# Optimization experiments

Hardware: AMD Instinct MI355X
Metric: run time of the kernel (lower is better)

Reference implementation:

```python
import jax, jax.numpy as jnp
import numpy as np

B, T, C = 4, 2048, 1024
H = 16
HD = C // H


def setup_inputs() -> dict:
    key = jax.random.key(0)
    k1, k2, k3 = jax.random.split(key, 3)
    x = jax.random.normal(k1, (B, T, C), dtype=jnp.float32)
    w_qkv = jax.random.normal(k2, (C, 3 * C), dtype=jnp.float32) * (C ** -0.5)
    w_proj = jax.random.normal(k3, (C, C), dtype=jnp.float32) * (C ** -0.5)
    b_proj = jnp.zeros((C,), dtype=jnp.float32)
    return {"x": x, "w_qkv": w_qkv, "w_proj": w_proj, "b_proj": b_proj}


def reference(x, w_qkv, w_proj, b_proj):
    Bd, Td, Cd = x.shape
    scale = HD ** -0.5
    qkv = x @ w_qkv  # [B,T,3C]
    q, k, v = jnp.split(qkv, 3, axis=-1)
    # [B,H,T,HD]
    q = q.reshape(Bd, Td, H, HD).transpose(0, 2, 1, 3)
    k = k.reshape(Bd, Td, H, HD).transpose(0, 2, 1, 3)
    v = v.reshape(Bd, Td, H, HD).transpose(0, 2, 1, 3)
    att = jnp.einsum('bhqd,bhkd->bhqk', q, k) * scale
    causal = jnp.triu(jnp.ones((Td, Td), dtype=bool), k=1)
    att = jnp.where(causal, -jnp.inf, att)
    att = jax.nn.softmax(att, axis=-1)
    y = jnp.einsum('bhqk,bhkd->bhqd', att, v)
    y = y.transpose(0, 2, 1, 3).reshape(Bd, Td, Cd)
    return y @ w_proj + b_proj
```

## Files before the change

kernel.cpp:

```cpp
#include <hip/hip_runtime.h>

typedef unsigned short u16;
typedef __attribute__((ext_vector_type(8))) short short8;
typedef __attribute__((ext_vector_type(4))) short short4v;
typedef __attribute__((ext_vector_type(4))) float floatx4;
typedef __attribute__((ext_vector_type(4))) unsigned short ushort4v;

#define B_ 4
#define T_ 2048
#define C_ 1024
#define H_ 16
#define HD_ 64

template <bool V> struct BC { static constexpr bool value = V; };

static __device__ __forceinline__ u16 f2bf(float f) {
  union { float f; unsigned int i; } c; c.f = f;
  unsigned int u = c.i;
  return (u16)((u + 0x7FFFu + ((u >> 16) & 1u)) >> 16);
}
static __device__ __forceinline__ unsigned pk2(float lo, float hi) {
  union { float f; unsigned u; } a, b; a.f = hi; b.f = lo;
  return __builtin_amdgcn_perm(a.u, b.u, 0x07060302u);
}
static __device__ __forceinline__ unsigned pk2r(float lo, float hi) {
  return (unsigned)f2bf(lo) | ((unsigned)f2bf(hi) << 16);
}

static __device__ __forceinline__ void gload16(const u16* g, u16* l) {
  __builtin_amdgcn_global_load_lds(
      (const __attribute__((address_space(1))) unsigned int*)(g),
      (__attribute__((address_space(3))) unsigned int*)(l), 16, 0, 0);
}

__global__ __launch_bounds__(256) void prep_k(const float* __restrict__ x,
                                              const float* __restrict__ w_qkv,
                                              const float* __restrict__ w_proj,
                                              u16* __restrict__ xbf,
                                              u16* __restrict__ wqkvT,
                                              u16* __restrict__ wprojT) {
  const int bid = blockIdx.x;
  if (bid < 8192) {
    const int i = bid * 256 + threadIdx.x;
    const float4 f = ((const float4*)x)[i];
    ushort4v o;
    o.x = f2bf(f.x); o.y = f2bf(f.y); o.z = f2bf(f.z); o.w = f2bf(f.w);
    *(ushort4v*)(xbf + (size_t)i * 4) = o;
    return;
  }
  __shared__ u16 tile[32][33];
  const float* in;
  u16* out;
  int R, Cc, tb;
  if (bid < 11264) {
    in = w_qkv; out = wqkvT; R = C_; Cc = 3 * C_; tb = bid - 8192;
  } else {
    in = w_proj; out = wprojT; R = C_; Cc = C_; tb = bid - 11264;
  }
  const int tpr = Cc / 32;
  const int bx = (tb % tpr) * 32;
  const int by = (tb / tpr) * 32;
  const int tx = threadIdx.x & 31;
  const int ty = threadIdx.x >> 5;
  #pragma unroll
  for (int i = ty; i < 32; i += 8)
    tile[i][tx] = f2bf(in[(size_t)(by + i) * Cc + bx + tx]);
  __syncthreads();
  #pragma unroll
  for (int i = ty; i < 32; i += 8)
    out[(size_t)(bx + i) * R + by + tx] = tile[tx][i];
}

template <int MODE, int NT>
__global__ __launch_bounds__(256) void gemm_bt(const u16* __restrict__ A,
                                               const u16* __restrict__ Bt,
                                               u16* __restrict__ outb,
                                               u16* __restrict__ outv,
                                               float* __restrict__ outf,
                                               const float* __restrict__ bias,
                                               int M, int N, int K) {
  __shared__ __align__(16) u16 lds[8192 + NT * 2048];
  const int bid = blockIdx.x;
  const int s = bid >> 3;
  const int tM = ((bid & 7) * 8 + (s & 7)) * 128;
  const int tN = (s >> 3) * (NT * 32);
  const int tid = threadIdx.x;
  const int wave = tid >> 6;
  const int lane = tid & 63;
  const int lr = lane & 15;
  const int quad = lane >> 4;
  const int wm = (wave >> 1) * 64;
  const int wn = (wave & 1) * (NT * 16);

  const int srow = lane >> 2;
  const int skofs = ((lane & 3) ^ ((lane >> 3) & 3)) * 8;

  const floatx4 zf = {0.f, 0.f, 0.f, 0.f};
  floatx4 acc[4][NT];
  #pragma unroll
  for (int i = 0; i < 4; i++)
    #pragma unroll
    for (int j = 0; j < NT; j++) acc[i][j] = zf;

  const int csw = (lr >> 1) & 3;

  for (int k0 = 0; k0 < K; k0 += 64) {
    __syncthreads();
    #pragma unroll
    for (int half = 0; half < 2; half++) {
      const int kk = k0 + half * 32;
      #pragma unroll
      for (int j = 0; j < 2; j++) {
        const int seg = wave * 2 + j;
        const int row = seg * 16 + srow;
        gload16(A + (size_t)(tM + row) * K + kk + skofs, &lds[half * 4096 + seg * 512]);
      }
      #pragma unroll
      for (int j = 0; j < NT / 2; j++) {
        const int seg = wave * (NT / 2) + j;
        const int row = seg * 16 + srow;
        gload16(Bt + (size_t)(tN + row) * K + kk + skofs,
                &lds[8192 + half * (NT * 1024) + seg * 512]);
      }
    }
    __syncthreads();

    #pragma unroll
    for (int half = 0; half < 2; half++) {
      short8 af[4], bfr[NT];
      #pragma unroll
      for (int mt = 0; mt < 4; mt++)
        af[mt] = *(const short8*)(&lds[half * 4096 + (wm + mt * 16 + lr) * 32 + ((quad ^ csw) * 8)]);
      #pragma unroll
      for (int nt = 0; nt < NT; nt++)
        bfr[nt] = *(const short8*)(&lds[8192 + half * (NT * 1024) + (wn + nt * 16 + lr) * 32 + ((quad ^ csw) * 8)]);
      #pragma unroll
      for (int mt = 0; mt < 4; mt++)
        #pragma unroll
        for (int nt = 0; nt < NT; nt++)
          acc[mt][nt] = __builtin_amdgcn_mfma_f32_16x16x32_bf16(af[mt], bfr[nt],
                                                                acc[mt][nt], 0, 0, 0);
    }
  }

  if (MODE == 1 && tN >= 2 * C_) {
    const int b = tM >> 11;
    const int t0 = tM & (T_ - 1);
    const int h0 = (tN - 2 * C_) >> 6;
    #pragma unroll
    for (int pass = 0; pass < 2; pass++) {
      __syncthreads();
      if ((wave & 1) == pass) {
        #pragma unroll
        for (int nt = 0; nt < NT; nt++) {
          const int nr = nt * 16 + lr;
          #pragma unroll
          for (int mt = 0; mt < 4; mt++) {
            const int mr = wm + mt * 16 + quad * 4;
            *(unsigned*)(&lds[nr * 136 + mr]) = pk2r(acc[mt][nt][0], acc[mt][nt][1]);
            *(unsigned*)(&lds[nr * 136 + mr + 2]) = pk2r(acc[mt][nt][2], acc[mt][nt][3]);
          }
        }
      }
      __syncthreads();
      const int bh = b * H_ + h0 + pass;
      u16* vbase = outv + (size_t)bh * HD_ * T_ + t0;
      #pragma unroll
      for (int i = 0; i < 4; i++) {
        const int c = tid + i * 256;
        const int nr = c >> 4, m8 = (c & 15) * 8;
        const short8 v = *(const short8*)(&lds[nr * 136 + m8]);
        *(short8*)(vbase + (size_t)nr * T_ + m8) = v;
      }
    }
    return;
  }

  #pragma unroll
  for (int mt = 0; mt < 4; mt++) {
    const int m0 = tM + wm + mt * 16 + quad * 4;
    #pragma unroll
    for (int nt = 0; nt < NT; nt++) {
      const int n = tN + wn + nt * 16 + lr;
      #pragma unroll
      for (int r = 0; r < 4; r++) {
        const float v = acc[mt][nt][r];
        const size_t m = (size_t)(m0 + r);
        if (MODE == 2) __builtin_nontemporal_store(v + bias[n], &outf[m * N + n]);
        else           outb[m * N + n] = f2bf(v);
      }
    }
  }
}

__global__ __launch_bounds__(256, 4) void attn_k(const u16* __restrict__ qkv,
                                                 const u16* __restrict__ vt,
                                                 u16* __restrict__ y) {
  __shared__ __align__(16) u16 Ks[64 * 64];
  __shared__ __align__(16) u16 Vs[64 * 64];
  const int bid = blockIdx.x;
  const int s = bid >> 3;
  const int qp = s >> 3;
  const int bh = ((s & 7) << 3) | (bid & 7);
  const int b = bh >> 4, h = bh & 15;
  const int tid = threadIdx.x;
  const int wave = tid >> 6;
  const int lane = tid & 63;
  const int lr = lane & 15;
  const int quad = lane >> 4;
  const int qtA = qp, qtB = 31 - qp;

  const int srow = lane >> 3;
  const int skofs = ((lane & 7) ^ ((lane >> 3) & 7)) * 8;
  const int gsw = lr & 7;

  const size_t RS = 3 * C_;
  const u16* qcol = qkv + (size_t)b * T_ * RS + h * HD_;
  const u16* kcol = qcol + C_;

  const size_t qrA = (size_t)(qtA * 64 + wave * 16 + lr) * RS;
  const size_t qrB = (size_t)(qtB * 64 + wave * 16 + lr) * RS;
  const short8 aq0A = *(const short8*)(qcol + qrA + quad * 8);
  const short8 aq1A = *(const short8*)(qcol + qrA + 32 + quad * 8);
  const short8 aq0B = *(const short8*)(qcol + qrB + quad * 8);
  const short8 aq1B = *(const short8*)(qcol + qrB + 32 + quad * 8);

  const floatx4 zf = {0.f, 0.f, 0.f, 0.f};
  const float C1 = 0.125f * 1.44269504f;
  const float C2 = -16.0f * 1.44269504f;
  const short8 vones = {16256, 16256, 16256, 16256, 16256, 16256, 16256, 16256};

  floatx4 accA[4], accB[4];
  floatx4 accSA = zf, accSB = zf;
  #pragma unroll
  for (int i = 0; i < 4; i++) { accA[i] = zf; accB[i] = zf; }

  auto stage = [&](int kt) {
    __syncthreads();
    #pragma unroll
    for (int j = 0; j < 2; j++) {
      const int seg = wave * 2 + j;
      const int row = seg * 8 + srow;
      gload16(kcol + (size_t)(kt * 64 + row) * RS + skofs, &Ks[seg * 512]);
      gload16(vt + ((size_t)bh * HD_ + row) * T_ + kt * 64 + skofs, &Vs[seg * 512]);
    }
    __syncthreads();
  };

  auto core = [&](auto WA, auto DA, auto DB) {
    constexpr bool wA = decltype(WA)::value;
    constexpr bool dA = decltype(DA)::value;
    constexpr bool dB = decltype(DB)::value;
    float peA[4][4], peB[4][4];
    #pragma unroll
    for (int nt = 0; nt < 4; nt++) {
      const short8 bk0 =
          *(const short8*)(&Ks[(nt * 16 + lr) * 64 + ((quad ^ gsw) * 8)]);
      const short8 bk1 =
          *(const short8*)(&Ks[(nt * 16 + lr) * 64 + (((quad + 4) ^ gsw) * 8)]);
      {
        floatx4 st = __builtin_amdgcn_mfma_f32_16x16x32_bf16(
            bk1, aq1B,
            __builtin_amdgcn_mfma_f32_16x16x32_bf16(bk0, aq0B, zf, 0, 0, 0),
            0, 0, 0);
        #pragma unroll
        for (int r = 0; r < 4; r++) {
          float pe = __builtin_amdgcn_exp2f(fmaf(st[r], C1, C2));
          if constexpr (dB)
            if (nt * 16 + quad * 4 + r > wave * 16 + lr) pe = 0.f;
          peB[nt][r] = pe;
        }
      }
      if constexpr (wA) {
        floatx4 st = __builtin_amdgcn_mfma_f32_16x16x32_bf16(
            bk1, aq1A,
            __builtin_amdgcn_mfma_f32_16x16x32_bf16(bk0, aq0A, zf, 0, 0, 0),
            0, 0, 0);
        #pragma unroll
        for (int r = 0; r < 4; r++) {
          float pe = __builtin_amdgcn_exp2f(fmaf(st[r], C1, C2));
          if constexpr (dA)
            if (nt * 16 + quad * 4 + r > wave * 16 + lr) pe = 0.f;
          peA[nt][r] = pe;
        }
      }
    }

    short8 pB[2], pA[2];
    #pragma unroll
    for (int h2 = 0; h2 < 2; h2++) {
      union { unsigned u[4]; short8 s8; } w;
      w.u[0] = pk2(peB[2 * h2][0], peB[2 * h2][1]);
      w.u[1] = pk2(peB[2 * h2][2], peB[2 * h2][3]);
      w.u[2] = pk2(peB[2 * h2 + 1][0], peB[2 * h2 + 1][1]);
      w.u[3] = pk2(peB[2 * h2 + 1][2], peB[2 * h2 + 1][3]);
      pB[h2] = w.s8;
    }
    if constexpr (wA) {
      #pragma unroll
      for (int h2 = 0; h2 < 2; h2++) {
        union { unsigned u[4]; short8 s8; } w;
        w.u[0] = pk2(peA[2 * h2][0], peA[2 * h2][1]);
        w.u[1] = pk2(peA[2 * h2][2], peA[2 * h2][3]);
        w.u[2] = pk2(peA[2 * h2 + 1][0], peA[2 * h2 + 1][1]);
        w.u[3] = pk2(peA[2 * h2 + 1][2], peA[2 * h2 + 1][3]);
        pA[h2] = w.s8;
      }
    }

    #pragma unroll
    for (int h2 = 0; h2 < 2; h2++) {
      accSB = __builtin_amdgcn_mfma_f32_16x16x32_bf16(vones, pB[h2], accSB, 0, 0, 0);
      if constexpr (wA)
        accSA = __builtin_amdgcn_mfma_f32_16x16x32_bf16(vones, pA[h2], accSA, 0, 0, 0);
      #pragma unroll
      for (int dt = 0; dt < 4; dt++) {
        const int base = (dt * 16 + lr) * 64;
        const int cl = h2 * 4 + (quad >> 1);
        const int off_lo = ((cl ^ gsw) * 8) + (quad & 1) * 4;
        const int off_hi = (((cl + 2) ^ gsw) * 8) + (quad & 1) * 4;
        const short4v vlo = *(const short4v*)(&Vs[base + off_lo]);
        const short4v vhi = *(const short4v*)(&Vs[base + off_hi]);
        const short8 av = __builtin_shufflevector(vlo, vhi, 0, 1, 2, 3, 4, 5, 6, 7);
        accB[dt] = __builtin_amdgcn_mfma_f32_16x16x32_bf16(av, pB[h2], accB[dt], 0, 0, 0);
        if constexpr (wA)
          accA[dt] = __builtin_amdgcn_mfma_f32_16x16x32_bf16(av, pA[h2], accA[dt], 0, 0, 0);
      }
    }
  };

  for (int kt = 0; kt < qtA; kt++) { stage(kt); core(BC<true>{}, BC<false>{}, BC<false>{}); }
  stage(qtA); core(BC<true>{}, BC<true>{}, BC<false>{});
  for (int kt = qtA + 1; kt < qtB; kt++) { stage(kt); core(BC<false>{}, BC<false>{}, BC<false>{}); }
  stage(qtB); core(BC<false>{}, BC<false>{}, BC<true>{});

  #pragma unroll
  for (int ph = 0; ph < 2; ph++) {
    const int qt = ph ? qtB : qtA;
    const floatx4* acc = ph ? accB : accA;
    const float inv = 1.f / (ph ? accSB[0] : accSA[0]);
    const int qg = qt * 64 + wave * 16 + lr;
    u16* yrow = y + ((size_t)(b * T_ + qg)) * C_ + h * HD_;
    #pragma unroll
    for (int dt = 0; dt < 4; dt++) {
      ushort4v o;
      #pragma unroll
      for (int r = 0; r < 4; r++) o[r] = f2bf(acc[dt][r] * inv);
      *(ushort4v*)(yrow + dt * 16 + quad * 4) = o;
    }
  }
}

extern "C" void kernel_launch(void* const* d_in, const int* in_sizes, int n_in,
                              void* d_out, int out_size, void* d_ws, size_t ws_size,
                              hipStream_t stream) {
  const float* x      = (const float*)d_in[0];
  const float* w_qkv  = (const float*)d_in[1];
  const float* w_proj = (const float*)d_in[2];
  const float* b_proj = (const float*)d_in[3];
  float* out = (float*)d_out;

  u16* ws = (u16*)d_ws;
  const size_t SZ = (size_t)B_ * T_ * C_;
  u16* xbf    = ws;
  u16* wqkvT  = xbf + SZ;
  u16* wprojT = wqkvT + (size_t)3 * C_ * C_;
  u16* qkvw   = wprojT + (size_t)C_ * C_;
  u16* vtw    = qkvw + 3 * SZ;
  u16* yw     = xbf;

  prep_k<<<12288, 256, 0, stream>>>(x, w_qkv, w_proj, xbf, wqkvT, wprojT);
  gemm_bt<1, 4><<<1536, 256, 0, stream>>>(
      xbf, wqkvT, qkvw, vtw, nullptr, nullptr, B_ * T_, 3 * C_, C_);
  attn_k<<<1024, 256, 0, stream>>>(qkvw, vtw, yw);
  gemm_bt<2, 2><<<1024, 256, 0, stream>>>(
      yw, wprojT, nullptr, nullptr, out, b_proj, B_ * T_, C_, C_);
}
```

Before: 239.0 us.

## Rewrite projection GEMMs as 512-thread 128x256 tiles with 4-stage LDS pipeline

Both projection GEMMs now use a new kernel with 512 threads and 128x256 output tiles. It runs a 4-buffer asynchronous global-to-LDS pipeline with explicit vmcnt waits and one barrier per k-step, and raises wave priority around the MFMA block. The aim is to hide global load latency behind compute and to get more reuse per tile than the old single-buffered 64-wide k loop with two syncthreads per step. The V-transpose epilogue now writes through an XOR-swizzled LDS layout. The costs are higher LDS use (96 KB) and fewer blocks, 256 for the output projection, which may underfill the GPU.

```diff
diff --git a/kernel.cpp b/kernel.cpp
--- a/kernel.cpp
+++ b/kernel.cpp
@@ -13,6 +13,7 @@
 #define HD_ 64
 
 template <bool V> struct BC { static constexpr bool value = V; };
+template <int N> struct ICN { static constexpr int v = N; };
 
 static __device__ __forceinline__ u16 f2bf(float f) {
   union { float f; unsigned int i; } c; c.f = f;
@@ -71,123 +72,142 @@
     out[(size_t)(bx + i) * R + by + tx] = tile[tx][i];
 }
 
-template <int MODE, int NT>
-__global__ __launch_bounds__(256) void gemm_bt(const u16* __restrict__ A,
-                                               const u16* __restrict__ Bt,
-                                               u16* __restrict__ outb,
-                                               u16* __restrict__ outv,
-                                               float* __restrict__ outf,
-                                               const float* __restrict__ bias,
-                                               int M, int N, int K) {
-  __shared__ __align__(16) u16 lds[8192 + NT * 2048];
+template <int MODE>
+__global__ __launch_bounds__(512, 2) void gemm8p(const u16* __restrict__ A,
+                                                 const u16* __restrict__ Bt,
+                                                 u16* __restrict__ outb,
+                                                 u16* __restrict__ outv,
+                                                 float* __restrict__ outf,
+                                                 const float* __restrict__ bias,
+                                                 int M, int N, int K) {
+  __shared__ __align__(16) u16 lds[49152];
   const int bid = blockIdx.x;
-  const int s = bid >> 3;
-  const int tM = ((bid & 7) * 8 + (s & 7)) * 128;
-  const int tN = (s >> 3) * (NT * 32);
+  const int xcd = bid & 7;
+  const int loc = bid >> 3;
+  const int tM = (xcd * 8 + (loc & 7)) * 128;
+  const int tN = (loc >> 3) * 256;
   const int tid = threadIdx.x;
   const int wave = tid >> 6;
   const int lane = tid & 63;
   const int lr = lane & 15;
   const int quad = lane >> 4;
-  const int wm = (wave >> 1) * 64;
-  const int wn = (wave & 1) * (NT * 16);
-
-  const int srow = lane >> 2;
+  const int wm = wave >> 2;
+  const int wn = wave & 3;
+  const int csw = (lr >> 1) & 3;
+  const int arow = wave * 16 + (lane >> 2);
   const int skofs = ((lane & 3) ^ ((lane >> 3) & 3)) * 8;
+  const int KT = K >> 5;
 
   const floatx4 zf = {0.f, 0.f, 0.f, 0.f};
-  floatx4 acc[4][NT];
+  floatx4 acc[4][4];
   #pragma unroll
   for (int i = 0; i < 4; i++)
     #pragma unroll
-    for (int j = 0; j < NT; j++) acc[i][j] = zf;
-
-  const int csw = (lr >> 1) & 3;
-
-  for (int k0 = 0; k0 < K; k0 += 64) {
-    __syncthreads();
-    #pragma unroll
-    for (int half = 0; half < 2; half++) {
-      const int kk = k0 + half * 32;
-      #pragma unroll
-      for (int j = 0; j < 2; j++) {
-        const int seg = wave * 2 + j;
-        const int row = seg * 16 + srow;
-        gload16(A + (size_t)(tM + row) * K + kk + skofs, &lds[half * 4096 + seg * 512]);
-      }
-      #pragma unroll
-      for (int j = 0; j < NT / 2; j++) {
-        const int seg = wave * (NT / 2) + j;
-        const int row = seg * 16 + srow;
-        gload16(Bt + (size_t)(tN + row) * K + kk + skofs,
-                &lds[8192 + half * (NT * 1024) + seg * 512]);
-      }
-    }
-    __syncthreads();
-
-    #pragma unroll
-    for (int half = 0; half < 2; half++) {
-      short8 af[4], bfr[NT];
-      #pragma unroll
-      for (int mt = 0; mt < 4; mt++)
-        af[mt] = *(const short8*)(&lds[half * 4096 + (wm + mt * 16 + lr) * 32 + ((quad ^ csw) * 8)]);
-      #pragma unroll
-      for (int nt = 0; nt < NT; nt++)
-        bfr[nt] = *(const short8*)(&lds[8192 + half * (NT * 1024) + (wn + nt * 16 + lr) * 32 + ((quad ^ csw) * 8)]);
-      #pragma unroll
-      for (int mt = 0; mt < 4; mt++)
-        #pragma unroll
-        for (int nt = 0; nt < NT; nt++)
-          acc[mt][nt] = __builtin_amdgcn_mfma_f32_16x16x32_bf16(af[mt], bfr[nt],
-                                                                acc[mt][nt], 0, 0, 0);
-    }
-  }
-
-  if (MODE == 1 && tN >= 2 * C_) {
-    const int b = tM >> 11;
-    const int t0 = tM & (T_ - 1);
-    const int h0 = (tN - 2 * C_) >> 6;
-    #pragma unroll
-    for (int pass = 0; pass < 2; pass++) {
-      __syncthreads();
-      if ((wave & 1) == pass) {
-        #pragma unroll
-        for (int nt = 0; nt < NT; nt++) {
-          const int nr = nt * 16 + lr;
-          #pragma unroll
-          for (int mt = 0; mt < 4; mt++) {
-            const int mr = wm + mt * 16 + quad * 4;
-            *(unsigned*)(&lds[nr * 136 + mr]) = pk2r(acc[mt][nt][0], acc[mt][nt][1]);
-            *(unsigned*)(&lds[nr * 136 + mr + 2]) = pk2r(acc[mt][nt][2], acc[mt][nt][3]);
-          }
+    for (int j = 0; j < 4; j++) acc[i][j] = zf;
+
+  auto stage = [&](int t) {
+    const int buf = t & 3;
+    const int kk = t * 32;
+    gload16(A + (size_t)(tM + arow) * K + kk + skofs,
+            &lds[buf * 4096 + wave * 512]);
+    gload16(Bt + (size_t)(tN + arow) * K + kk + skofs,
+            &lds[16384 + buf * 8192 + wave * 512]);
+    gload16(Bt + (size_t)(tN + 128 + arow) * K + kk + skofs,
+            &lds[16384 + buf * 8192 + 4096 + wave * 512]);
+  };
+
+  auto ktile = [&](int t, auto VM) {
+    const int buf = t & 3;
+    const u16* lA = &lds[buf * 4096];
+    const u16* lB = &lds[16384 + buf * 8192];
+    short8 af[4], bfr[4];
+    #pragma unroll
+    for (int mt = 0; mt < 4; mt++)
+      af[mt] = *(const short8*)(&lA[(wm * 64 + mt * 16 + lr) * 32 + ((quad ^ csw) * 8)]);
+    #pragma unroll
+    for (int nt = 0; nt < 4; nt++)
+      bfr[nt] = *(const short8*)(&lB[(wn * 64 + nt * 16 + lr) * 32 + ((quad ^ csw) * 8)]);
+    if (t + 3 < KT) stage(t + 3);
+    asm volatile("s_waitcnt lgkmcnt(0)" ::: "memory");
+    __builtin_amdgcn_sched_barrier(0);
+    __builtin_amdgcn_s_setprio(1);
+    #pragma unroll
+    for (int mt = 0; mt < 4; mt++)
+      #pragma unroll
+      for (int nt = 0; nt < 4; nt++)
+        acc[mt][nt] = __builtin_amdgcn_mfma_f32_16x16x32_bf16(af[mt], bfr[nt],
+                                                              acc[mt][nt], 0, 0, 0);
+    __builtin_amdgcn_s_setprio(0);
+    __builtin_amdgcn_sched_barrier(0);
+    constexpr int vm = decltype(VM)::v;
+    if constexpr (vm == 6)
+      asm volatile("s_waitcnt vmcnt(6)\n\ts_barrier" ::: "memory");
+    else if constexpr (vm == 3)
+      asm volatile("s_waitcnt vmcnt(3)\n\ts_barrier" ::: "memory");
+    else if constexpr (vm == 0)
+      asm volatile("s_waitcnt vmcnt(0)\n\ts_barrier" ::: "memory");
+  };
+
+  stage(0); stage(1); stage(2);
+  asm volatile("s_waitcnt vmcnt(6)\n\ts_barrier" ::: "memory");
+
+  for (int t = 0; t < KT - 3; t++) ktile(t, ICN<6>{});
+  ktile(KT - 3, ICN<3>{});
+  ktile(KT - 2, ICN<0>{});
+  ktile(KT - 1, ICN<-1>{});
+
+  if constexpr (MODE == 1) {
+    if (tN >= 2 * C_) {
+      asm volatile("s_barrier" ::: "memory");
+      #pragma unroll
+      for (int mt = 0; mt < 4; mt++) {
+        const int t0 = wm * 64 + mt * 16 + quad * 4;
+        #pragma unroll
+        for (int nt = 0; nt < 4; nt++) {
+          const int vrow = wn * 64 + nt * 16 + lr;
+          u16* p = &lds[vrow * 128 + (((t0 >> 3) ^ (vrow & 7)) * 8) + (t0 & 7)];
+          *(unsigned*)(p)     = pk2r(acc[mt][nt][0], acc[mt][nt][1]);
+          *(unsigned*)(p + 2) = pk2r(acc[mt][nt][2], acc[mt][nt][3]);
         }
       }
-      __syncthreads();
-      const int bh = b * H_ + h0 + pass;
-      u16* vbase = outv + (size_t)bh * HD_ * T_ + t0;
-      #pragma unroll
-      for (int i = 0; i < 4; i++) {
-        const int c = tid + i * 256;
-        const int nr = c >> 4, m8 = (c & 15) * 8;
-        const short8 v = *(const short8*)(&lds[nr * 136 + m8]);
-        *(short8*)(vbase + (size_t)nr * T_ + m8) = v;
-      }
-    }
-    return;
-  }
-
-  #pragma unroll
-  for (int mt = 0; mt < 4; mt++) {
-    const int m0 = tM + wm + mt * 16 + quad * 4;
-    #pragma unroll
-    for (int nt = 0; nt < NT; nt++) {
-      const int n = tN + wn + nt * 16 + lr;
-      #pragma unroll
-      for (int r = 0; r < 4; r++) {
-        const float v = acc[mt][nt][r];
-        const size_t m = (size_t)(m0 + r);
-        if (MODE == 2) __builtin_nontemporal_store(v + bias[n], &outf[m * N + n]);
-        else           outb[m * N + n] = f2bf(v);
+      asm volatile("s_waitcnt lgkmcnt(0)\n\ts_barrier" ::: "memory");
+      const int b = tM >> 11;
+      const int t0b = tM & (T_ - 1);
+      const int h0 = (tN - 2 * C_) >> 6;
+      u16* vb = outv + (size_t)(b * H_ + h0) * HD_ * T_;
+      #pragma unroll
+      for (int i = 0; i < 8; i++) {
+        const int lin = tid + i * 512;
+        const int row = lin >> 4;
+        const int chv = lin & 15;
+        const short8 v = *(const short8*)(&lds[row * 128 + ((chv ^ (row & 7)) * 8)]);
+        *(short8*)(vb + (size_t)row * T_ + t0b + chv * 8) = v;
+      }
+      return;
+    }
+    #pragma unroll
+    for (int mt = 0; mt < 4; mt++) {
+      const int m0 = tM + wm * 64 + mt * 16 + quad * 4;
+      #pragma unroll
+      for (int nt = 0; nt < 4; nt++) {
+        const int n = tN + wn * 64 + nt * 16 + lr;
+        #pragma unroll
+        for (int r = 0; r < 4; r++)
+          outb[(size_t)(m0 + r) * N + n] = f2bf(acc[mt][nt][r]);
+      }
+    }
+  } else {
+    #pragma unroll
+    for (int mt = 0; mt < 4; mt++) {
+      const int m0 = tM + wm * 64 + mt * 16 + quad * 4;
+      #pragma unroll
+      for (int nt = 0; nt < 4; nt++) {
+        const int n = tN + wn * 64 + nt * 16 + lr;
+        const float bv = bias[n];
+        #pragma unroll
+        for (int r = 0; r < 4; r++)
+          __builtin_nontemporal_store(acc[mt][nt][r] + bv,
+                                      &outf[(size_t)(m0 + r) * N + n]);
       }
     }
   }
@@ -370,9 +390,9 @@
   u16* yw     = xbf;
 
   prep_k<<<12288, 256, 0, stream>>>(x, w_qkv, w_proj, xbf, wqkvT, wprojT);
-  gemm_bt<1, 4><<<1536, 256, 0, stream>>>(
+  gemm8p<1><<<768, 512, 0, stream>>>(
       xbf, wqkvT, qkvw, vtw, nullptr, nullptr, B_ * T_, 3 * C_, C_);
   attn_k<<<1024, 256, 0, stream>>>(qkvw, vtw, yw);
-  gemm_bt<2, 2><<<1024, 256, 0, stream>>>(
+  gemm8p<2><<<256, 512, 0, stream>>>(
       yw, wprojT, nullptr, nullptr, out, b_proj, B_ * T_, C_, C_);
 }
```

Measured after the change: 235.7 us. No clear change (-1.4%).
